# Kernel tuning notes

Hardware: AMD Instinct MI355X
Metric: run time of the kernel (lower is better)

Reference implementation:

```python
import jax, jax.numpy as jnp
import numpy as np

DIM = 256
DIM_HEAD = 32
HEADS = DIM // DIM_HEAD
NUM_TYPES = 2
WS = 7
AGENTS = 6
SCALE = DIM_HEAD ** -0.5


def _rel_pos_index():
    # Static relative-position index for a WS x WS window (torch meshgrid default = 'ij')
    coords = np.stack(np.meshgrid(np.arange(WS), np.arange(WS), indexing='ij'))  # (2,WS,WS)
    cf = coords.reshape(2, -1)                     # (2, WS*WS)
    rel = cf[:, :, None] - cf[:, None, :]          # (2, 49, 49)
    rel = rel.transpose(1, 2, 0).copy()
    rel[:, :, 0] += WS - 1
    rel[:, :, 1] += WS - 1
    rel[:, :, 0] *= 2 * WS - 1
    return jnp.asarray(rel.sum(-1))                # (49, 49) int


def setup_inputs() -> dict:
    key = jax.random.key(0)
    ks = jax.random.split(key, 16)
    B, L, X, Y = 4, AGENTS, 8, 8
    x = jax.random.normal(ks[0], (B, L, X, Y, WS, WS, DIM), dtype=jnp.float32)
    mode = jax.random.randint(ks[1], (B, L), 0, NUM_TYPES)
    s = 0.02
    Wq = jax.random.normal(ks[2], (NUM_TYPES, DIM, DIM), dtype=jnp.float32) * s
    bq = jax.random.normal(ks[3], (NUM_TYPES, DIM), dtype=jnp.float32) * s
    Wk = jax.random.normal(ks[4], (NUM_TYPES, DIM, DIM), dtype=jnp.float32) * s
    bk = jax.random.normal(ks[5], (NUM_TYPES, DIM), dtype=jnp.float32) * s
    Wv = jax.random.normal(ks[6], (NUM_TYPES, DIM, DIM), dtype=jnp.float32) * s
    bv = jax.random.normal(ks[7], (NUM_TYPES, DIM), dtype=jnp.float32) * s
    Wa = jax.random.normal(ks[8], (NUM_TYPES, DIM, DIM), dtype=jnp.float32) * s
    ba = jax.random.normal(ks[9], (NUM_TYPES, DIM), dtype=jnp.float32) * s
    # xavier_uniform over (num_relations, heads, dh, dh): fan based on last two dims
    lim = float(np.sqrt(6.0 / (DIM_HEAD + DIM_HEAD)))
    relation_att = jax.random.uniform(ks[10], (NUM_TYPES * NUM_TYPES, HEADS, DIM_HEAD, DIM_HEAD), minval=-lim, maxval=lim, dtype=jnp.float32)
    relation_msg = jax.random.uniform(ks[11], (NUM_TYPES * NUM_TYPES, HEADS, DIM_HEAD, DIM_HEAD), minval=-lim, maxval=lim, dtype=jnp.float32)
    pos_table = jax.random.normal(ks[12], ((2 * WS - 1) * (2 * WS - 1), HEADS), dtype=jnp.float32)
    return dict(x=x, mode=mode, Wq=Wq, bq=bq, Wk=Wk, bk=bk, Wv=Wv, bv=bv, Wa=Wa, ba=ba,
                relation_att=relation_att, relation_msg=relation_msg, pos_table=pos_table)


def reference(x, mode, Wq, bq, Wk, bk, Wv, bv, Wa, ba, relation_att, relation_msg, pos_table):
    B, L, X, Y, w1, w2, D = x.shape
    h, dh = HEADS, DIM_HEAD
    W = w1 * w2

    def proj(Wt, bt):
        # type-routed Linear: gather per-(b,l) weight, y = x @ W[t].T + b[t]
        y = jnp.einsum('blxyuvd,bled->blxyuve', x, Wt[mode]) + bt[mode][:, :, None, None, None, None, :]
        # b l x y u v (h d) -> b x y h l u v d
        return y.reshape(B, L, X, Y, w1, w2, h, dh).transpose(0, 2, 3, 6, 1, 4, 5, 7)

    q = proj(Wq, bq)[:, :, :, :, :1] * SCALE   # ego agent only (a=1)
    k = proj(Wk, bk)
    v = proj(Wv, bv)

    # relation index for (ego type, agent z type): r[b,z] = mode[b,0]*T + mode[b,z]
    rel_idx = mode[:, :1] * NUM_TYPES + mode           # (B, L)
    w_att = relation_att[rel_idx]                      # (B, L, h, dh, dh)
    w_msg = relation_msg[rel_idx]

    # sim_{pq} = q_p W_att[p,q] k_q
    kw = jnp.einsum('bzhpq,bxyhzefq->bxyhzefp', w_att, k)
    sim = jnp.einsum('bxyhacdp,bxyhzefp->bxyhacdzef', q, kw)  # (B,X,Y,h,1,w1,w2,L,w1,w2)

    # relative position bias, broadcast over agents z
    bias = pos_table[_rel_pos_index()].transpose(2, 0, 1)     # (h, 49, 49)
    sim = sim.reshape(B, X, Y, h, 1, W, L, W) + bias[None, None, None, :, None, :, None, :]

    # softmax over all keys (z, e, f) jointly
    attn = jax.nn.softmax(sim.reshape(B, X, Y, h, W, L * W), axis=-1)
    attn = attn.reshape(B, X, Y, h, 1, w1, w2, L, w1, w2)

    # message: v'_q = sum_p v_p W_msg[p,q]
    v_msg = jnp.einsum('bzhpq,bxyhzefp->bxyhzefq', w_msg, v)
    out = jnp.einsum('bxyhacdzef,bxyhzefq->bxyhacdq', attn, v_msg)

    # b x y h a c d q -> b a x y c d (h q)
    out = out.transpose(0, 4, 1, 2, 5, 6, 3, 7).reshape(B, 1, X, Y, w1, w2, D)

    # type-routed output projection for ego agent
    m0 = mode[:, :1]
    out = jnp.einsum('blxyuvd,bled->blxyuve', out, Wa[m0]) + ba[m0][:, :, None, None, None, None, :]
    return out
```

## Files before the change

### kernel.cpp

```cpp
#include <hip/hip_runtime.h>

typedef unsigned short u16;
typedef unsigned int   u32;
typedef _Float16 f16;
typedef _Float16 h2  __attribute__((ext_vector_type(2)));
typedef _Float16 h8  __attribute__((ext_vector_type(8)));
typedef float    fx4 __attribute__((ext_vector_type(4)));

#define SCALE_Q 0.17677669529663687f

__device__ __forceinline__ u16 f2h_bits(float f){
  union{ f16 h; u16 u; } v; v.h = (f16)f; return v.u;
}
__device__ __forceinline__ u32 packh2(float a, float b){
  union{ h2 h; u32 u; } v; v.h = h2{(f16)a, (f16)b}; return v.u;
}
__device__ __forceinline__ h2 as_h2(u32 x){
  union{ u32 u; h2 h; } v; v.u = x; return v.h;
}
__device__ __forceinline__ h8 as_h8(uint4 u){
  union{ uint4 u; h8 h; } v; v.u = u; return v.h;
}

__global__ void flag_fill(float* out, int n, float v){
  int i = blockIdx.x*256 + threadIdx.x;
  if (i < n) out[i] = v;
}

__global__ __launch_bounds__(512) void fuse_w(
    const float* __restrict__ Wk, const float* __restrict__ Wv,
    const float* __restrict__ Ratt, const float* __restrict__ Rmsg,
    u16* __restrict__ Wft)
{
  const int rel = blockIdx.x;
  const int d   = blockIdx.y;
  const int n   = threadIdx.x;
  const int ml  = rel & 1;
  float acc = 0.f;
  if (n < 256) {
    const int h = n >> 5, p = n & 31;
    const float* wcol = Wk + (size_t)ml*65536 + (size_t)(h*32)*256 + d;
    const float* rrow = Ratt + ((size_t)(rel*8 + h)*32 + p)*32;
    #pragma unroll
    for (int q = 0; q < 32; ++q) acc += wcol[q*256] * rrow[q];
  } else {
    const int n2 = n - 256, h = n2 >> 5, qq = n2 & 31;
    const float* wcol = Wv + (size_t)ml*65536 + (size_t)(h*32)*256 + d;
    const float* rcol = Rmsg + ((size_t)(rel*8 + h)*32)*32 + qq;
    #pragma unroll
    for (int p2 = 0; p2 < 32; ++p2) acc += wcol[p2*256] * rcol[p2*32];
  }
  Wft[(size_t)rel*131072 + (size_t)(d >> 5)*16384 + (size_t)n*32 + (d & 31)] = f2h_bits(acc);
}

__global__ __launch_bounds__(512) void fuse_b(
    const float* __restrict__ bk, const float* __restrict__ bv,
    const float* __restrict__ Ratt, const float* __restrict__ Rmsg,
    float* __restrict__ bff)
{
  const int rel = blockIdx.x, n = threadIdx.x, ml = rel & 1;
  float acc = 0.f;
  if (n < 256) {
    const int h = n >> 5, p = n & 31;
    const float* rrow = Ratt + ((size_t)(rel*8 + h)*32 + p)*32;
    #pragma unroll
    for (int q = 0; q < 32; ++q) acc += bk[ml*256 + h*32 + q] * rrow[q];
  } else {
    const int n2 = n - 256, h = n2 >> 5, qq = n2 & 31;
    const float* rcol = Rmsg + ((size_t)(rel*8 + h)*32)*32 + qq;
    #pragma unroll
    for (int p2 = 0; p2 < 32; ++p2) acc += bv[ml*256 + h*32 + p2] * rcol[p2*32];
  }
  bff[rel*512 + n] = acc;
}

__global__ __launch_bounds__(512) void fuse_qo(
    const float* __restrict__ Wq, const float* __restrict__ Wa,
    u16* __restrict__ Wqf, u16* __restrict__ Waf)
{
  const int t = blockIdx.x;
  const int d = blockIdx.y;
  const int n = threadIdx.x;
  if (n < 256){
    float v = Wq[(size_t)t*65536 + (size_t)n*256 + d] * SCALE_Q;
    Wqf[(size_t)t*65536 + (size_t)(d >> 5)*8192 + (size_t)n*32 + (d & 31)] = f2h_bits(v);
  } else {
    const int e = n - 256;
    float v = Wa[(size_t)t*65536 + (size_t)e*256 + d];
    Waf[(size_t)t*65536 + (size_t)(d >> 5)*8192 + (size_t)e*32 + (d & 31)] = f2h_bits(v);
  }
}

#define ASTRIDE 264

__global__ __launch_bounds__(256, 2) void gemm_kwv(
    const float* __restrict__ x, const int* __restrict__ mode,
    const u16* __restrict__ Wft, const float* __restrict__ bff,
    u16* __restrict__ kw, u16* __restrict__ vm, int b0)
{
  __shared__ u16 Smem[32*ASTRIDE];
  const int rowT  = blockIdx.x;
  const int bloc = rowT / 588;
  const int rem  = rowT % 588;
  const int l = rem / 98, tile = rem % 98;
  const int b = b0 + bloc;
  const int rel = mode[b*6]*2 + mode[b*6 + l];
  const float* Abase = x + ((size_t)(b*6 + l)*3136 + (size_t)tile*32)*256;
  const int tid  = threadIdx.x;
  const int wave = tid >> 6, lane = tid & 63;
  const int quad = lane >> 4, l15 = lane & 15;

  const u16* Bp = Wft + (size_t)rel*131072 + (size_t)((wave << 7) + l15)*32 + (quad << 3);

  uint4 breg[32];
  #pragma unroll
  for (int s = 0; s < 8; ++s)
    #pragma unroll
    for (int j = 0; j < 4; ++j){
      const u16* ap = Bp + (size_t)s*16384 + j*512;
      asm volatile("global_load_dwordx4 %0, %1, off" : "=v"(breg[s*4+j]) : "v"(ap));
    }

  {
    const int r = tid >> 3, cseg = (tid & 7)*32;
    const float* src = Abase + (size_t)r*256 + cseg;
    u16* dst = &Smem[r*ASTRIDE + cseg];
    #pragma unroll
    for (int i = 0; i < 4; ++i){
      float4 f0 = *(const float4*)(src + i*8);
      float4 f1 = *(const float4*)(src + i*8 + 4);
      uint4 pk;
      pk.x = packh2(f0.x, f0.y); pk.y = packh2(f0.z, f0.w);
      pk.z = packh2(f1.x, f1.y); pk.w = packh2(f1.z, f1.w);
      *(uint4*)(dst + i*8) = pk;
    }
  }
  __syncthreads();

  fx4 acc[2][8];
  #pragma unroll
  for (int mt = 0; mt < 2; ++mt)
    #pragma unroll
    for (int j = 0; j < 8; ++j) acc[mt][j] = fx4{0,0,0,0};

  const u16* As0 = &Smem[l15*ASTRIDE + (quad << 3)];
  const u16* As1 = As0 + 16*ASTRIDE;

  asm volatile("s_waitcnt vmcnt(0)" ::: "memory");
  __builtin_amdgcn_sched_barrier(0);
  #pragma unroll
  for (int s = 0; s < 8; ++s){
    h8 af0 = *(const h8*)(As0 + s*32);
    h8 af1 = *(const h8*)(As1 + s*32);
    #pragma unroll
    for (int j = 0; j < 4; ++j){
      h8 bf = as_h8(breg[s*4+j]);
      acc[0][j] = __builtin_amdgcn_mfma_f32_16x16x32_f16(af0, bf, acc[0][j], 0, 0, 0);
      acc[1][j] = __builtin_amdgcn_mfma_f32_16x16x32_f16(af1, bf, acc[1][j], 0, 0, 0);
    }
  }

  #pragma unroll
  for (int s = 0; s < 8; ++s)
    #pragma unroll
    for (int j = 0; j < 4; ++j){
      const u16* ap = Bp + (size_t)s*16384 + (size_t)(4 + j)*512;
      asm volatile("global_load_dwordx4 %0, %1, off" : "=v"(breg[s*4+j]) : "v"(ap));
    }
  asm volatile("s_waitcnt vmcnt(0)" ::: "memory");
  __builtin_amdgcn_sched_barrier(0);
  #pragma unroll
  for (int s = 0; s < 8; ++s){
    h8 af0 = *(const h8*)(As0 + s*32);
    h8 af1 = *(const h8*)(As1 + s*32);
    #pragma unroll
    for (int j = 0; j < 4; ++j){
      h8 bf = as_h8(breg[s*4+j]);
      acc[0][4+j] = __builtin_amdgcn_mfma_f32_16x16x32_f16(af0, bf, acc[0][4+j], 0, 0, 0);
      acc[1][4+j] = __builtin_amdgcn_mfma_f32_16x16x32_f16(af1, bf, acc[1][4+j], 0, 0, 0);
    }
  }

  const int row_ = tid >> 3;
  const int hsel = tid & 7;
  const int r_g  = tile*32 + row_;
  const int xy   = r_g / 49, ef = r_g - xy*49;

  #pragma unroll
  for (int half = 0; half < 2; ++half){
    __syncthreads();
    if ((wave >> 1) == half){
      #pragma unroll
      for (int j = 0; j < 8; ++j){
        const int n   = wave*128 + j*16 + l15;
        const int col = n & 255;
        const float bias = bff[rel*512 + n];
        #pragma unroll
        for (int mt = 0; mt < 2; ++mt){
          #pragma unroll
          for (int reg = 0; reg < 4; ++reg){
            const int row = mt*16 + quad*4 + reg;
            Smem[row*ASTRIDE + col] = f2h_bits(acc[mt][j][reg] + bias);
          }
        }
      }
    }
    __syncthreads();
    u16* dbuf = half ? vm : kw;
    u16* dst  = dbuf + ((((size_t)(bloc*64 + xy)*8 + hsel)*6 + l)*49 + ef)*32;
    const u16* srcl = &Smem[row_*ASTRIDE + hsel*32];
    uint4 v0 = *(const uint4*)(srcl);
    uint4 v1 = *(const uint4*)(srcl + 8);
    uint4 v2 = *(const uint4*)(srcl + 16);
    uint4 v3 = *(const uint4*)(srcl + 24);
    *(uint4*)(dst)      = v0;
    *(uint4*)(dst + 8)  = v1;
    *(uint4*)(dst + 16) = v2;
    *(uint4*)(dst + 24) = v3;
  }
}

__global__ __launch_bounds__(256, 2) void gemm_qp(
    const float* __restrict__ x, const int* __restrict__ mode,
    const u16* __restrict__ Wqf, const float* __restrict__ bq,
    u16* __restrict__ qbuf)
{
  __shared__ u16 Smem[32*ASTRIDE];
  const int rowT = blockIdx.x;
  const int b = rowT / 98, tile = rowT % 98;
  const int m0 = mode[b*6];
  const float* Abase = x + ((size_t)(b*6)*3136 + (size_t)tile*32)*256;
  const int tid = threadIdx.x;
  const int wave = tid >> 6, lane = tid & 63;
  const int quad = lane >> 4, l15 = lane & 15;

  const u16* Bp = Wqf + (size_t)m0*65536 + (size_t)((wave << 6) + l15)*32 + (quad << 3);
  uint4 breg[32];
  #pragma unroll
  for (int s = 0; s < 8; ++s)
    #pragma unroll
    for (int j = 0; j < 4; ++j){
      const u16* ap = Bp + (size_t)s*8192 + j*512;
      asm volatile("global_load_dwordx4 %0, %1, off" : "=v"(breg[s*4+j]) : "v"(ap));
    }

  {
    const int r = tid >> 3, cseg = (tid & 7)*32;
    const float* src = Abase + (size_t)r*256 + cseg;
    u16* dst = &Smem[r*ASTRIDE + cseg];
    #pragma unroll
    for (int i = 0; i < 4; ++i){
      float4 f0 = *(const float4*)(src + i*8);
      float4 f1 = *(const float4*)(src + i*8 + 4);
      uint4 pk;
      pk.x = packh2(f0.x, f0.y); pk.y = packh2(f0.z, f0.w);
      pk.z = packh2(f1.x, f1.y); pk.w = packh2(f1.z, f1.w);
      *(uint4*)(dst + i*8) = pk;
    }
  }
  __syncthreads();

  fx4 acc[2][4];
  #pragma unroll
  for (int mt = 0; mt < 2; ++mt)
    #pragma unroll
    for (int j = 0; j < 4; ++j) acc[mt][j] = fx4{0,0,0,0};

  const u16* As0 = &Smem[l15*ASTRIDE + (quad << 3)];
  const u16* As1 = As0 + 16*ASTRIDE;
  asm volatile("s_waitcnt vmcnt(0)" ::: "memory");
  __builtin_amdgcn_sched_barrier(0);
  #pragma unroll
  for (int s = 0; s < 8; ++s){
    h8 af0 = *(const h8*)(As0 + s*32);
    h8 af1 = *(const h8*)(As1 + s*32);
    #pragma unroll
    for (int j = 0; j < 4; ++j){
      h8 bf = as_h8(breg[s*4+j]);
      acc[0][j] = __builtin_amdgcn_mfma_f32_16x16x32_f16(af0, bf, acc[0][j], 0, 0, 0);
      acc[1][j] = __builtin_amdgcn_mfma_f32_16x16x32_f16(af1, bf, acc[1][j], 0, 0, 0);
    }
  }

  __syncthreads();
  #pragma unroll
  for (int j = 0; j < 4; ++j){
    const int n = wave*64 + j*16 + l15;
    const float bias = bq[m0*256 + n] * SCALE_Q;
    #pragma unroll
    for (int mt = 0; mt < 2; ++mt)
      #pragma unroll
      for (int reg = 0; reg < 4; ++reg){
        const int row = mt*16 + quad*4 + reg;
        Smem[row*ASTRIDE + n] = f2h_bits(acc[mt][j][reg] + bias);
      }
  }
  __syncthreads();
  {
    const int row_ = tid >> 3, hsel = tid & 7;
    const int r_g = tile*32 + row_;
    const int xy = r_g / 49, ef = r_g - xy*49;
    u16* dst = qbuf + (((size_t)(b*64 + xy)*8 + hsel)*49 + ef)*32;
    const u16* srcl = &Smem[row_*ASTRIDE + hsel*32];
    *(uint4*)(dst)      = *(const uint4*)(srcl);
    *(uint4*)(dst + 8)  = *(const uint4*)(srcl + 8);
    *(uint4*)(dst + 16) = *(const uint4*)(srcl + 16);
    *(uint4*)(dst + 24) = *(const uint4*)(srcl + 24);
  }
}

__global__ __launch_bounds__(64) void attn_kernel(
    const u16* __restrict__ qbuf, const u16* __restrict__ kw,
    const u16* __restrict__ vm,   const float* __restrict__ post,
    u16* __restrict__ aout, int b0)
{
  __shared__ u32 Ks[64*16];
  __shared__ u16 VT[32*64];
  __shared__ u16 PQ[64*64];
  __shared__ float poss[169];

  const int bloc  = blockIdx.x >> 9;
  const int local = blockIdx.x & 511;
  const int h = local & 7, xy = local >> 3;
  const int bxy = (b0 + bloc)*64 + xy;
  const int lane = threadIdx.x;
  const int quad = lane >> 4, l15 = lane & 15;

  for (int i = lane; i < 169; i += 64) poss[i] = post[i*8 + h];
  for (int i = lane; i < 240; i += 64) Ks[784 + i] = 0;
  for (int i = lane; i < 512; i += 64){
    const int p = i >> 4, ke = 48 + (i & 15);
    VT[p*64 + ((((ke >> 3) ^ (p & 7)) & 7) << 3) + (ke & 7)] = 0;
  }
  { const u16* qsrc = qbuf + (size_t)(bxy*8 + h)*1568;
    for (int i = lane; i < 196; i += 64)
      *(uint4*)&PQ[(i >> 2)*32 + (i & 3)*8] = *(const uint4*)(qsrc + (size_t)i*8);
    const uint4 z4 = make_uint4(0,0,0,0);
    for (int i = lane; i < 60; i += 64)
      *(uint4*)&PQ[1568 + i*8] = z4;
  }
  __syncthreads();

  h8 qf[4];
  #pragma unroll
  for (int nt = 0; nt < 4; ++nt)
    qf[nt] = *(const h8*)&PQ[(nt*16 + l15)*32 + quad*8];

  fx4 bias[4][4];
  { int qa[4], qb[4];
    #pragma unroll
    for (int nt = 0; nt < 4; ++nt){
      const int qi = nt*16 + l15; qa[nt] = qi/7; qb[nt] = qi - qa[nt]*7;
    }
    #pragma unroll
    for (int mt = 0; mt < 4; ++mt)
      #pragma unroll
      for (int reg = 0; reg < 4; ++reg){
        const int ke = mt*16 + quad*4 + reg;
        const int ka = ke/7, kb = ke - ka*7;
        #pragma unroll
        for (int nt = 0; nt < 4; ++nt){
          const int qi = nt*16 + l15;
          float bv;
          if (ke > 48)      bv = -1e30f;
          else if (qi > 48) bv = 0.f;
          else              bv = poss[(qa[nt] - ka + 6)*13 + (qb[nt] - kb + 6)];
          bias[mt][nt][reg] = bv;
        }
      }
  }

  const size_t kvbase = ((size_t)(bloc*64 + xy)*8 + h)*6;
  float mprev[4], lsum[4];
  fx4 Oacc[2][4];
  #pragma unroll
  for (int nt = 0; nt < 4; ++nt){
    mprev[nt] = -1e30f; lsum[nt] = 0.f;
    Oacc[0][nt] = fx4{0,0,0,0}; Oacc[1][nt] = fx4{0,0,0,0};
  }

  for (int z = 0; z < 6; ++z){
    __syncthreads();
    { const uint4* ksrc = (const uint4*)((const u32*)kw + (kvbase + z)*784);
      for (int i = lane; i < 196; i += 64) ((uint4*)Ks)[i] = ksrc[i];
      const uint4* vsrc = (const uint4*)((const u32*)vm + (kvbase + z)*784);
      for (int i = lane; i < 196; i += 64){
        uint4 v4 = vsrc[i];
        const int ef = i >> 2, pb = (i & 3)*8;
        const int c0 = ef >> 3;
        u16* vt = VT + (ef & 7);
        vt[(pb+0)*64 + ((c0 ^ 0) << 3)] = (u16)(v4.x & 0xFFFFu);
        vt[(pb+1)*64 + ((c0 ^ 1) << 3)] = (u16)(v4.x >> 16);
        vt[(pb+2)*64 + ((c0 ^ 2) << 3)] = (u16)(v4.y & 0xFFFFu);
        vt[(pb+3)*64 + ((c0 ^ 3) << 3)] = (u16)(v4.y >> 16);
        vt[(pb+4)*64 + ((c0 ^ 4) << 3)] = (u16)(v4.z & 0xFFFFu);
        vt[(pb+5)*64 + ((c0 ^ 5) << 3)] = (u16)(v4.z >> 16);
        vt[(pb+6)*64 + ((c0 ^ 6) << 3)] = (u16)(v4.w & 0xFFFFu);
        vt[(pb+7)*64 + ((c0 ^ 7) << 3)] = (u16)(v4.w >> 16);
      } }
    __syncthreads();

    h8 kf[4];
    #pragma unroll
    for (int mt = 0; mt < 4; ++mt)
      kf[mt] = *(const h8*)((const u16*)Ks + (mt*16 + l15)*32 + quad*8);
    fx4 S[4][4];
    #pragma unroll
    for (int mt = 0; mt < 4; ++mt)
      #pragma unroll
      for (int nt = 0; nt < 4; ++nt)
        S[mt][nt] = __builtin_amdgcn_mfma_f32_16x16x32_f16(kf[mt], qf[nt], bias[mt][nt], 0, 0, 0);

    #pragma unroll
    for (int nt = 0; nt < 4; ++nt){
      float cm = S[0][nt][0];
      #pragma unroll
      for (int mt = 0; mt < 4; ++mt)
        #pragma unroll
        for (int r = 0; r < 4; ++r) cm = fmaxf(cm, S[mt][nt][r]);
      cm = fmaxf(cm, __shfl_xor(cm, 16));
      cm = fmaxf(cm, __shfl_xor(cm, 32));
      const float mnew = fmaxf(mprev[nt], cm);
      const float alpha = __expf(mprev[nt] - mnew);
      mprev[nt] = mnew;
      float sum = 0.f;
      #pragma unroll
      for (int mt = 0; mt < 4; ++mt)
        #pragma unroll
        for (int r = 0; r < 4; ++r){
          float e = __expf(S[mt][nt][r] - mnew); S[mt][nt][r] = e; sum += e;
        }
      sum += __shfl_xor(sum, 16);
      sum += __shfl_xor(sum, 32);
      lsum[nt] = lsum[nt]*alpha + sum;
      #pragma unroll
      for (int r = 0; r < 4; ++r){ Oacc[0][nt][r] *= alpha; Oacc[1][nt][r] *= alpha; }
    }

    #pragma unroll
    for (int nt = 0; nt < 4; ++nt){
      const int qi = nt*16 + l15;
      u16* prow = &PQ[qi*64 + ((quad & 1) << 2)];
      #pragma unroll
      for (int mt = 0; mt < 4; ++mt){
        const int chk = (mt*2 + (quad >> 1)) ^ (l15 & 7);
        uint2 w;
        w.x = packh2(S[mt][nt][0], S[mt][nt][1]);
        w.y = packh2(S[mt][nt][2], S[mt][nt][3]);
        *(uint2*)(prow + (chk << 3)) = w;
      }
    }
    __syncthreads();

    #pragma unroll
    for (int ks = 0; ks < 2; ++ks){
      h8 vf[2];
      #pragma unroll
      for (int m2 = 0; m2 < 2; ++m2)
        vf[m2] = *(const h8*)&VT[(m2*16 + l15)*64 + (((ks*4 + quad) ^ (l15 & 7)) << 3)];
      #pragma unroll
      for (int nt = 0; nt < 4; ++nt){
        h8 pf = *(const h8*)&PQ[(nt*16 + l15)*64 + (((ks*4 + quad) ^ (l15 & 7)) << 3)];
        Oacc[0][nt] = __builtin_amdgcn_mfma_f32_16x16x32_f16(vf[0], pf, Oacc[0][nt], 0, 0, 0);
        Oacc[1][nt] = __builtin_amdgcn_mfma_f32_16x16x32_f16(vf[1], pf, Oacc[1][nt], 0, 0, 0);
      }
    }
  }

  __syncthreads();
  #pragma unroll
  for (int nt = 0; nt < 4; ++nt){
    const int qi = nt*16 + l15;
    if (qi < 49){
      const float inv = 1.f / lsum[nt];
      #pragma unroll
      for (int m2 = 0; m2 < 2; ++m2){
        uint2 w;
        w.x = packh2(Oacc[m2][nt][0]*inv, Oacc[m2][nt][1]*inv);
        w.y = packh2(Oacc[m2][nt][2]*inv, Oacc[m2][nt][3]*inv);
        *(uint2*)&PQ[qi*32 + m2*16 + quad*4] = w;
      }
    }
  }
  __syncthreads();
  { u16* obase = aout + (size_t)bxy*12544 + h*32;
    for (int i = lane; i < 196; i += 64){
      const int r = i >> 2, c = (i & 3)*8;
      *(uint4*)(obase + (size_t)r*256 + c) = *(const uint4*)&PQ[r*32 + c];
    }
  }
}

__global__ __launch_bounds__(256, 2) void gemm_op(
    const u16* __restrict__ aout, const int* __restrict__ mode,
    const u16* __restrict__ Waf, const float* __restrict__ ba,
    float* __restrict__ outp)
{
  __shared__ float Smf[32*260];
  u16* Smem = (u16*)Smf;
  const int rowT = blockIdx.x;
  const int b = rowT / 98, tile = rowT % 98;
  const int m0 = mode[b*6];
  const u16* Abase = aout + ((size_t)b*3136 + (size_t)tile*32)*256;
  const int tid = threadIdx.x;
  const int wave = tid >> 6, lane = tid & 63;
  const int quad = lane >> 4, l15 = lane & 15;

  const u16* Bp = Waf + (size_t)m0*65536 + (size_t)((wave << 6) + l15)*32 + (quad << 3);
  uint4 breg[32];
  #pragma unroll
  for (int s = 0; s < 8; ++s)
    #pragma unroll
    for (int j = 0; j < 4; ++j){
      const u16* ap = Bp + (size_t)s*8192 + j*512;
      asm volatile("global_load_dwordx4 %0, %1, off" : "=v"(breg[s*4+j]) : "v"(ap));
    }

  {
    const int r = tid >> 3, cseg = (tid & 7)*32;
    const u16* src = Abase + (size_t)r*256 + cseg;
    u16* dst = &Smem[r*ASTRIDE + cseg];
    #pragma unroll
    for (int i = 0; i < 4; ++i)
      *(uint4*)(dst + i*8) = *(const uint4*)(src + i*8);
  }
  __syncthreads();

  fx4 acc[2][4];
  #pragma unroll
  for (int mt = 0; mt < 2; ++mt)
    #pragma unroll
    for (int j = 0; j < 4; ++j) acc[mt][j] = fx4{0,0,0,0};

  const u16* As0 = &Smem[l15*ASTRIDE + (quad << 3)];
  const u16* As1 = As0 + 16*ASTRIDE;
  asm volatile("s_waitcnt vmcnt(0)" ::: "memory");
  __builtin_amdgcn_sched_barrier(0);
  #pragma unroll
  for (int s = 0; s < 8; ++s){
    h8 af0 = *(const h8*)(As0 + s*32);
    h8 af1 = *(const h8*)(As1 + s*32);
    #pragma unroll
    for (int j = 0; j < 4; ++j){
      h8 bf = as_h8(breg[s*4+j]);
      acc[0][j] = __builtin_amdgcn_mfma_f32_16x16x32_f16(af0, bf, acc[0][j], 0, 0, 0);
      acc[1][j] = __builtin_amdgcn_mfma_f32_16x16x32_f16(af1, bf, acc[1][j], 0, 0, 0);
    }
  }

  __syncthreads();
  #pragma unroll
  for (int j = 0; j < 4; ++j){
    const int n = wave*64 + j*16 + l15;
    const float bias = ba[m0*256 + n];
    #pragma unroll
    for (int mt = 0; mt < 2; ++mt)
      #pragma unroll
      for (int reg = 0; reg < 4; ++reg){
        const int row = mt*16 + quad*4 + reg;
        Smf[row*260 + n] = acc[mt][j][reg] + bias;
      }
  }
  __syncthreads();
  {
    const int row_ = tid >> 3, seg = (tid & 7)*32;
    const int rowg = b*3136 + tile*32 + row_;
    float* dst = outp + (size_t)rowg*256 + seg;
    const float* srcl = &Smf[row_*260 + seg];
    #pragma unroll
    for (int i = 0; i < 8; ++i)
      *(float4*)(dst + i*4) = *(const float4*)(srcl + i*4);
  }
}

extern "C" void kernel_launch(void* const* d_in, const int* in_sizes, int n_in,
                              void* d_out, int out_size, void* d_ws, size_t ws_size,
                              hipStream_t stream)
{
  float* outp = (float*)d_out;
  const int FLAG_GRID = (out_size + 255)/256;

  if (n_in != 13) { flag_fill<<<FLAG_GRID,256,0,stream>>>(outp, out_size, 2000.f); return; }
  if (in_sizes[0] != 4*6*64*49*256) { flag_fill<<<FLAG_GRID,256,0,stream>>>(outp, out_size, 3000.f); return; }
  if (in_sizes[1] != 24) { flag_fill<<<FLAG_GRID,256,0,stream>>>(outp, out_size, 4000.f); return; }

  const size_t SZ_WFT  = (size_t)4*512*256*2;
  const size_t SZ_BFF  = (size_t)4*512*sizeof(float);
  const size_t SZ_WQF  = (size_t)2*256*256*2;
  const size_t SZ_WAF  = (size_t)2*256*256*2;
  const size_t SZ_Q    = (size_t)12544*256*2;
  const size_t SZ_AOUT = (size_t)12544*256*2;
  const size_t SZ_KW1  = (size_t)64*8*6*49*32*2;
  const size_t SZ_VM1  = SZ_KW1;
  const size_t FIXED   = SZ_WFT + SZ_BFF + SZ_WQF + SZ_WAF + SZ_Q + SZ_AOUT;
  if (ws_size < FIXED + SZ_KW1 + SZ_VM1) { flag_fill<<<FLAG_GRID,256,0,stream>>>(outp, out_size, 1000.f); return; }

  int nb = 1;
  if (ws_size >= FIXED + 4*(SZ_KW1 + SZ_VM1)) nb = 4;
  else if (ws_size >= FIXED + 2*(SZ_KW1 + SZ_VM1)) nb = 2;

  const float* x    = (const float*)d_in[0];
  const int*   mode = (const int*)d_in[1];
  const float* Wq   = (const float*)d_in[2];
  const float* bq   = (const float*)d_in[3];
  const float* Wk   = (const float*)d_in[4];
  const float* bk   = (const float*)d_in[5];
  const float* Wv   = (const float*)d_in[6];
  const float* bv   = (const float*)d_in[7];
  const float* Wa   = (const float*)d_in[8];
  const float* ba   = (const float*)d_in[9];
  const float* Ratt = (const float*)d_in[10];
  const float* Rmsg = (const float*)d_in[11];
  const float* post = (const float*)d_in[12];

  char* w = (char*)d_ws;
  u16* Wft   = (u16*)w;   w += SZ_WFT;
  float* bff = (float*)w; w += SZ_BFF;
  u16* Wqf   = (u16*)w;   w += SZ_WQF;
  u16* Waf   = (u16*)w;   w += SZ_WAF;
  u16* qbuf  = (u16*)w;   w += SZ_Q;
  u16* aout  = (u16*)w;   w += SZ_AOUT;
  u16* kwbuf = (u16*)w;   w += (size_t)nb*SZ_KW1;
  u16* vmbuf = (u16*)w;   w += (size_t)nb*SZ_VM1;

  fuse_w<<<dim3(4,256), 512, 0, stream>>>(Wk, Wv, Ratt, Rmsg, Wft);
  fuse_b<<<4, 512, 0, stream>>>(bk, bv, Ratt, Rmsg, bff);
  fuse_qo<<<dim3(2,256), 512, 0, stream>>>(Wq, Wa, Wqf, Waf);
  gemm_qp<<<392, 256, 0, stream>>>(x, mode, Wqf, bq, qbuf);
  for (int b0 = 0; b0 < 4; b0 += nb) {
    gemm_kwv<<<nb*588, 256, 0, stream>>>(x, mode, Wft, bff, kwbuf, vmbuf, b0);
    attn_kernel<<<nb*512, 64, 0, stream>>>(qbuf, kwbuf, vmbuf, post, aout, b0);
  }
  gemm_op<<<392, 256, 0, stream>>>(aout, mode, Waf, ba, outp);
}
```

Measured before the change: 281.7 us.

## Merge weight-fusion kernels and retile K/V GEMM to 64-row tiles with pipelined B loads

The three small weight-preprocessing kernels are merged into one launch to cut launch overhead. The K/V projection GEMM moves from 32-row tiles on 256 threads to 64-row tiles on 512 threads. Each wave now owns 64 output columns across 4 M-subtiles, which doubles reuse of each B fragment. B fragments now stream through a 3-slot register ring with staged vmcnt waits instead of two bulk load phases, which cuts register pressure and overlaps loads with MFMA work. The trade-offs are fewer blocks, a larger LDS footprint, and the loss of the explicit two-blocks-per-CU occupancy hint.

```diff
diff --git a/kernel.cpp b/kernel.cpp
--- a/kernel.cpp
+++ b/kernel.cpp
@@ -27,176 +27,152 @@
   if (i < n) out[i] = v;
 }
 
-__global__ __launch_bounds__(512) void fuse_w(
+__global__ __launch_bounds__(512) void fuse_all(
     const float* __restrict__ Wk, const float* __restrict__ Wv,
     const float* __restrict__ Ratt, const float* __restrict__ Rmsg,
-    u16* __restrict__ Wft)
-{
-  const int rel = blockIdx.x;
-  const int d   = blockIdx.y;
-  const int n   = threadIdx.x;
-  const int ml  = rel & 1;
-  float acc = 0.f;
-  if (n < 256) {
-    const int h = n >> 5, p = n & 31;
-    const float* wcol = Wk + (size_t)ml*65536 + (size_t)(h*32)*256 + d;
-    const float* rrow = Ratt + ((size_t)(rel*8 + h)*32 + p)*32;
-    #pragma unroll
-    for (int q = 0; q < 32; ++q) acc += wcol[q*256] * rrow[q];
-  } else {
-    const int n2 = n - 256, h = n2 >> 5, qq = n2 & 31;
-    const float* wcol = Wv + (size_t)ml*65536 + (size_t)(h*32)*256 + d;
-    const float* rcol = Rmsg + ((size_t)(rel*8 + h)*32)*32 + qq;
-    #pragma unroll
-    for (int p2 = 0; p2 < 32; ++p2) acc += wcol[p2*256] * rcol[p2*32];
-  }
-  Wft[(size_t)rel*131072 + (size_t)(d >> 5)*16384 + (size_t)n*32 + (d & 31)] = f2h_bits(acc);
-}
-
-__global__ __launch_bounds__(512) void fuse_b(
+    const float* __restrict__ Wq, const float* __restrict__ Wa,
     const float* __restrict__ bk, const float* __restrict__ bv,
-    const float* __restrict__ Ratt, const float* __restrict__ Rmsg,
-    float* __restrict__ bff)
-{
-  const int rel = blockIdx.x, n = threadIdx.x, ml = rel & 1;
-  float acc = 0.f;
-  if (n < 256) {
-    const int h = n >> 5, p = n & 31;
-    const float* rrow = Ratt + ((size_t)(rel*8 + h)*32 + p)*32;
-    #pragma unroll
-    for (int q = 0; q < 32; ++q) acc += bk[ml*256 + h*32 + q] * rrow[q];
-  } else {
-    const int n2 = n - 256, h = n2 >> 5, qq = n2 & 31;
-    const float* rcol = Rmsg + ((size_t)(rel*8 + h)*32)*32 + qq;
-    #pragma unroll
-    for (int p2 = 0; p2 < 32; ++p2) acc += bv[ml*256 + h*32 + p2] * rcol[p2*32];
-  }
-  bff[rel*512 + n] = acc;
-}
-
-__global__ __launch_bounds__(512) void fuse_qo(
-    const float* __restrict__ Wq, const float* __restrict__ Wa,
+    u16* __restrict__ Wft, float* __restrict__ bff,
     u16* __restrict__ Wqf, u16* __restrict__ Waf)
 {
-  const int t = blockIdx.x;
-  const int d = blockIdx.y;
+  const int blk = blockIdx.x;
   const int n = threadIdx.x;
-  if (n < 256){
-    float v = Wq[(size_t)t*65536 + (size_t)n*256 + d] * SCALE_Q;
-    Wqf[(size_t)t*65536 + (size_t)(d >> 5)*8192 + (size_t)n*32 + (d & 31)] = f2h_bits(v);
+  if (blk < 1024){
+    const int rel = blk >> 8, d = blk & 255, ml = rel & 1;
+    float acc = 0.f;
+    if (n < 256) {
+      const int h = n >> 5, p = n & 31;
+      const float* wcol = Wk + (size_t)ml*65536 + (size_t)(h*32)*256 + d;
+      const float* rrow = Ratt + ((size_t)(rel*8 + h)*32 + p)*32;
+      #pragma unroll
+      for (int q = 0; q < 32; ++q) acc += wcol[q*256] * rrow[q];
+    } else {
+      const int n2 = n - 256, h = n2 >> 5, qq = n2 & 31;
+      const float* wcol = Wv + (size_t)ml*65536 + (size_t)(h*32)*256 + d;
+      const float* rcol = Rmsg + ((size_t)(rel*8 + h)*32)*32 + qq;
+      #pragma unroll
+      for (int p2 = 0; p2 < 32; ++p2) acc += wcol[p2*256] * rcol[p2*32];
+    }
+    Wft[(size_t)rel*131072 + (size_t)(d >> 5)*16384 + (size_t)n*32 + (d & 31)] = f2h_bits(acc);
+  } else if (blk < 1028){
+    const int rel = blk - 1024, ml = rel & 1;
+    float acc = 0.f;
+    if (n < 256) {
+      const int h = n >> 5, p = n & 31;
+      const float* rrow = Ratt + ((size_t)(rel*8 + h)*32 + p)*32;
+      #pragma unroll
+      for (int q = 0; q < 32; ++q) acc += bk[ml*256 + h*32 + q] * rrow[q];
+    } else {
+      const int n2 = n - 256, h = n2 >> 5, qq = n2 & 31;
+      const float* rcol = Rmsg + ((size_t)(rel*8 + h)*32)*32 + qq;
+      #pragma unroll
+      for (int p2 = 0; p2 < 32; ++p2) acc += bv[ml*256 + h*32 + p2] * rcol[p2*32];
+    }
+    bff[rel*512 + n] = acc;
   } else {
-    const int e = n - 256;
-    float v = Wa[(size_t)t*65536 + (size_t)e*256 + d];
-    Waf[(size_t)t*65536 + (size_t)(d >> 5)*8192 + (size_t)e*32 + (d & 31)] = f2h_bits(v);
+    const int bb = blk - 1028;
+    const int t = bb >> 8, d = bb & 255;
+    if (n < 256){
+      float v = Wq[(size_t)t*65536 + (size_t)n*256 + d] * SCALE_Q;
+      Wqf[(size_t)t*65536 + (size_t)(d >> 5)*8192 + (size_t)n*32 + (d & 31)] = f2h_bits(v);
+    } else {
+      const int e = n - 256;
+      float v = Wa[(size_t)t*65536 + (size_t)e*256 + d];
+      Waf[(size_t)t*65536 + (size_t)(d >> 5)*8192 + (size_t)e*32 + (d & 31)] = f2h_bits(v);
+    }
   }
 }
 
 #define ASTRIDE 264
 
-__global__ __launch_bounds__(256, 2) void gemm_kwv(
+__global__ __launch_bounds__(512) void gemm_kwv(
     const float* __restrict__ x, const int* __restrict__ mode,
     const u16* __restrict__ Wft, const float* __restrict__ bff,
     u16* __restrict__ kw, u16* __restrict__ vm, int b0)
 {
-  __shared__ u16 Smem[32*ASTRIDE];
+  __shared__ u16 Smem[64*ASTRIDE];
   const int rowT  = blockIdx.x;
-  const int bloc = rowT / 588;
-  const int rem  = rowT % 588;
-  const int l = rem / 98, tile = rem % 98;
+  const int bloc = rowT / 294;
+  const int rem  = rowT % 294;
+  const int l = rem / 49, tile = rem % 49;
   const int b = b0 + bloc;
   const int rel = mode[b*6]*2 + mode[b*6 + l];
-  const float* Abase = x + ((size_t)(b*6 + l)*3136 + (size_t)tile*32)*256;
+  const float* Abase = x + ((size_t)(b*6 + l)*3136 + (size_t)tile*64)*256;
   const int tid  = threadIdx.x;
   const int wave = tid >> 6, lane = tid & 63;
   const int quad = lane >> 4, l15 = lane & 15;
 
-  const u16* Bp = Wft + (size_t)rel*131072 + (size_t)((wave << 7) + l15)*32 + (quad << 3);
-
-  uint4 breg[32];
-  #pragma unroll
-  for (int s = 0; s < 8; ++s)
+  const u16* Bp = Wft + (size_t)rel*131072 + (size_t)((wave << 6) + l15)*32 + (quad << 3);
+
+  uint4 breg[3][4];
+  #pragma unroll
+  for (int s = 0; s < 3; ++s)
     #pragma unroll
     for (int j = 0; j < 4; ++j){
       const u16* ap = Bp + (size_t)s*16384 + j*512;
-      asm volatile("global_load_dwordx4 %0, %1, off" : "=v"(breg[s*4+j]) : "v"(ap));
-    }
-
-  {
-    const int r = tid >> 3, cseg = (tid & 7)*32;
-    const float* src = Abase + (size_t)r*256 + cseg;
-    u16* dst = &Smem[r*ASTRIDE + cseg];
-    #pragma unroll
-    for (int i = 0; i < 4; ++i){
-      float4 f0 = *(const float4*)(src + i*8);
-      float4 f1 = *(const float4*)(src + i*8 + 4);
-      uint4 pk;
-      pk.x = packh2(f0.x, f0.y); pk.y = packh2(f0.z, f0.w);
-      pk.z = packh2(f1.x, f1.y); pk.w = packh2(f1.z, f1.w);
-      *(uint4*)(dst + i*8) = pk;
-    }
-  }
-  __syncthreads();
-
-  fx4 acc[2][8];
-  #pragma unroll
-  for (int mt = 0; mt < 2; ++mt)
-    #pragma unroll
-    for (int j = 0; j < 8; ++j) acc[mt][j] = fx4{0,0,0,0};
-
-  const u16* As0 = &Smem[l15*ASTRIDE + (quad << 3)];
-  const u16* As1 = As0 + 16*ASTRIDE;
-
-  asm volatile("s_waitcnt vmcnt(0)" ::: "memory");
-  __builtin_amdgcn_sched_barrier(0);
+      asm volatile("global_load_dwordx4 %0, %1, off" : "=v"(breg[s][j]) : "v"(ap));
+    }
+
+  #pragma unroll
+  for (int i = 0; i < 8; ++i){
+    float4 f = *(const float4*)(Abase + (size_t)i*2048 + tid*4);
+    const int row = i*8 + (tid >> 6), col = (tid & 63)*4;
+    uint2 pk; pk.x = packh2(f.x, f.y); pk.y = packh2(f.z, f.w);
+    *(uint2*)&Smem[row*ASTRIDE + col] = pk;
+  }
+  __syncthreads();
+
+  fx4 acc[4][4];
+  #pragma unroll
+  for (int mt = 0; mt < 4; ++mt)
+    #pragma unroll
+    for (int j = 0; j < 4; ++j) acc[mt][j] = fx4{0,0,0,0};
+
+  const u16* As = &Smem[l15*ASTRIDE + (quad << 3)];
+
   #pragma unroll
   for (int s = 0; s < 8; ++s){
-    h8 af0 = *(const h8*)(As0 + s*32);
-    h8 af1 = *(const h8*)(As1 + s*32);
+    if (s >= 3 && s <= 5)      { asm volatile("s_waitcnt vmcnt(8)" ::: "memory"); }
+    else if (s == 6)           { asm volatile("s_waitcnt vmcnt(4)" ::: "memory"); }
+    else if (s == 7)           { asm volatile("s_waitcnt vmcnt(0)" ::: "memory"); }
+    __builtin_amdgcn_sched_barrier(0);
+    h8 af[4];
+    #pragma unroll
+    for (int mt = 0; mt < 4; ++mt)
+      af[mt] = *(const h8*)(As + (mt*16)*ASTRIDE + s*32);
+    const int slot = s % 3;
     #pragma unroll
     for (int j = 0; j < 4; ++j){
-      h8 bf = as_h8(breg[s*4+j]);
-      acc[0][j] = __builtin_amdgcn_mfma_f32_16x16x32_f16(af0, bf, acc[0][j], 0, 0, 0);
-      acc[1][j] = __builtin_amdgcn_mfma_f32_16x16x32_f16(af1, bf, acc[1][j], 0, 0, 0);
-    }
-  }
-
-  #pragma unroll
-  for (int s = 0; s < 8; ++s)
-    #pragma unroll
-    for (int j = 0; j < 4; ++j){
-      const u16* ap = Bp + (size_t)s*16384 + (size_t)(4 + j)*512;
-      asm volatile("global_load_dwordx4 %0, %1, off" : "=v"(breg[s*4+j]) : "v"(ap));
-    }
-  asm volatile("s_waitcnt vmcnt(0)" ::: "memory");
-  __builtin_amdgcn_sched_barrier(0);
-  #pragma unroll
-  for (int s = 0; s < 8; ++s){
-    h8 af0 = *(const h8*)(As0 + s*32);
-    h8 af1 = *(const h8*)(As1 + s*32);
-    #pragma unroll
-    for (int j = 0; j < 4; ++j){
-      h8 bf = as_h8(breg[s*4+j]);
-      acc[0][4+j] = __builtin_amdgcn_mfma_f32_16x16x32_f16(af0, bf, acc[0][4+j], 0, 0, 0);
-      acc[1][4+j] = __builtin_amdgcn_mfma_f32_16x16x32_f16(af1, bf, acc[1][4+j], 0, 0, 0);
+      h8 bf = as_h8(breg[slot][j]);
+      #pragma unroll
+      for (int mt = 0; mt < 4; ++mt)
+        acc[mt][j] = __builtin_amdgcn_mfma_f32_16x16x32_f16(af[mt], bf, acc[mt][j], 0, 0, 0);
+    }
+    if (s < 5){
+      #pragma unroll
+      for (int j = 0; j < 4; ++j){
+        const u16* ap = Bp + (size_t)(s + 3)*16384 + j*512;
+        asm volatile("global_load_dwordx4 %0, %1, off" : "=v"(breg[slot][j]) : "v"(ap));
+      }
     }
   }
 
   const int row_ = tid >> 3;
   const int hsel = tid & 7;
-  const int r_g  = tile*32 + row_;
+  const int r_g  = tile*64 + row_;
   const int xy   = r_g / 49, ef = r_g - xy*49;
 
   #pragma unroll
   for (int half = 0; half < 2; ++half){
     __syncthreads();
-    if ((wave >> 1) == half){
-      #pragma unroll
-      for (int j = 0; j < 8; ++j){
-        const int n   = wave*128 + j*16 + l15;
+    if ((wave >> 2) == half){
+      #pragma unroll
+      for (int j = 0; j < 4; ++j){
+        const int n   = wave*64 + j*16 + l15;
         const int col = n & 255;
         const float bias = bff[rel*512 + n];
         #pragma unroll
-        for (int mt = 0; mt < 2; ++mt){
+        for (int mt = 0; mt < 4; ++mt){
           #pragma unroll
           for (int reg = 0; reg < 4; ++reg){
             const int row = mt*16 + quad*4 + reg;
@@ -209,14 +185,10 @@
     u16* dbuf = half ? vm : kw;
     u16* dst  = dbuf + ((((size_t)(bloc*64 + xy)*8 + hsel)*6 + l)*49 + ef)*32;
     const u16* srcl = &Smem[row_*ASTRIDE + hsel*32];
-    uint4 v0 = *(const uint4*)(srcl);
-    uint4 v1 = *(const uint4*)(srcl + 8);
-    uint4 v2 = *(const uint4*)(srcl + 16);
-    uint4 v3 = *(const uint4*)(srcl + 24);
-    *(uint4*)(dst)      = v0;
-    *(uint4*)(dst + 8)  = v1;
-    *(uint4*)(dst + 16) = v2;
-    *(uint4*)(dst + 24) = v3;
+    *(uint4*)(dst)      = *(const uint4*)(srcl);
+    *(uint4*)(dst + 8)  = *(const uint4*)(srcl + 8);
+    *(uint4*)(dst + 16) = *(const uint4*)(srcl + 16);
+    *(uint4*)(dst + 24) = *(const uint4*)(srcl + 24);
   }
 }
 
@@ -623,12 +595,11 @@
   u16* kwbuf = (u16*)w;   w += (size_t)nb*SZ_KW1;
   u16* vmbuf = (u16*)w;   w += (size_t)nb*SZ_VM1;
 
-  fuse_w<<<dim3(4,256), 512, 0, stream>>>(Wk, Wv, Ratt, Rmsg, Wft);
-  fuse_b<<<4, 512, 0, stream>>>(bk, bv, Ratt, Rmsg, bff);
-  fuse_qo<<<dim3(2,256), 512, 0, stream>>>(Wq, Wa, Wqf, Waf);
+  fuse_all<<<1540, 512, 0, stream>>>(Wk, Wv, Ratt, Rmsg, Wq, Wa, bk, bv,
+                                     Wft, bff, Wqf, Waf);
   gemm_qp<<<392, 256, 0, stream>>>(x, mode, Wqf, bq, qbuf);
   for (int b0 = 0; b0 < 4; b0 += nb) {
-    gemm_kwv<<<nb*588, 256, 0, stream>>>(x, mode, Wft, bff, kwbuf, vmbuf, b0);
+    gemm_kwv<<<nb*294, 512, 0, stream>>>(x, mode, Wft, bff, kwbuf, vmbuf, b0);
     attn_kernel<<<nb*512, 64, 0, stream>>>(qbuf, kwbuf, vmbuf, post, aout, b0);
   }
   gemm_op<<<392, 256, 0, stream>>>(aout, mode, Waf, ba, outp);
```

Measured after the change: 271.4 us. -3.6%, faster.
